# Performance work log

Measured on AMD Instinct MI355X. Metric: run time of the kernel, lower is better.

## Reference

```python
import jax, jax.numpy as jnp
import numpy as np

B, S, D = 2, 2048, 2048
H, KVH = 32, 8
HD = D // H          # 64
N_REP = H // KVH     # 4
NEG = -1e9


def setup_inputs() -> dict:
    key = jax.random.key(0)
    ks = jax.random.split(key, 5)
    x = jax.random.normal(ks[0], (B, S, D), dtype=jnp.float32)
    std = 0.02
    wq = jax.random.normal(ks[1], (H * HD, D), dtype=jnp.float32) * std
    wk = jax.random.normal(ks[2], (KVH * HD, D), dtype=jnp.float32) * std
    wv = jax.random.normal(ks[3], (KVH * HD, D), dtype=jnp.float32) * std
    wo = jax.random.normal(ks[4], (D, H * HD), dtype=jnp.float32) * std
    # RoPE tables: (S, HD//2)
    inv_freq = 1.0 / (10000.0 ** (np.arange(0, HD, 2, dtype=np.float32) / HD))
    t = np.arange(S, dtype=np.float32)
    freqs = np.outer(t, inv_freq)
    freqs_cos = jnp.asarray(np.cos(freqs))
    freqs_sin = jnp.asarray(np.sin(freqs))
    # additive causal mask [1,1,S,S]
    causal = np.tril(np.ones((S, S), dtype=bool))
    mask = jnp.asarray(np.where(causal, 0.0, NEG).astype(np.float32))[None, None]
    return {"x": x, "wq": wq, "wk": wk, "wv": wv, "wo": wo,
            "freqs_cos": freqs_cos, "freqs_sin": freqs_sin, "mask": mask}


def _apply_rope(t, cos, sin):
    # t: [B,S,nh,HD]; cos/sin: [S, HD//2]
    tr = t.reshape(t.shape[:-1] + (HD // 2, 2))
    r, i = tr[..., 0], tr[..., 1]
    c = cos[None, :, None, :]
    s = sin[None, :, None, :]
    out_r = r * c - i * s
    out_i = r * s + i * c
    return jnp.stack([out_r, out_i], axis=-1).reshape(t.shape)


def reference(x, wq, wk, wv, wo, freqs_cos, freqs_sin, mask):
    b, s, _ = x.shape
    q = (x @ wq.T).reshape(b, s, H, HD)
    k = (x @ wk.T).reshape(b, s, KVH, HD)
    v = (x @ wv.T).reshape(b, s, KVH, HD)
    q = _apply_rope(q, freqs_cos, freqs_sin)
    k = _apply_rope(k, freqs_cos, freqs_sin)
    # repeat_kv (GQA expansion) then move heads forward: [B,H,S,HD]
    k = jnp.repeat(k, N_REP, axis=2)
    v = jnp.repeat(v, N_REP, axis=2)
    q = q.transpose(0, 2, 1, 3)
    k = k.transpose(0, 2, 1, 3)
    v = v.transpose(0, 2, 1, 3)
    scale = 1.0 / jnp.sqrt(jnp.float32(HD))
    scores = jnp.einsum("bhqd,bhkd->bhqk", q, k) * scale + mask[:, :, :s, :s]
    attn = jax.nn.softmax(scores, axis=-1)
    out = jnp.einsum("bhqk,bhkd->bhqd", attn, v)
    out = out.transpose(0, 2, 1, 3).reshape(b, s, H * HD)
    return out @ wo.T
```

## Files before the change

kernel.cpp:

```cpp
#include <hip/hip_runtime.h>
#include <hip/hip_bf16.h>
#include <stdint.h>


#define NEG_BIG (-1e9f)
#define SCALE_LOG2 0.18033688011112042f
#define DEFER_THR 10.0f

typedef __bf16 bf16x8 __attribute__((ext_vector_type(8)));
typedef float f32x4 __attribute__((ext_vector_type(4)));
typedef float f32x16 __attribute__((ext_vector_type(16)));
typedef uint16_t u16x8 __attribute__((ext_vector_type(8)));
typedef uint32_t u32x4 __attribute__((ext_vector_type(4)));

__device__ inline uint16_t f2bf(float x) {
    __hip_bfloat16 h = __float2bfloat16(x);
    return __builtin_bit_cast(uint16_t, h);
}
__device__ inline float bf2f(uint16_t u) {
    uint32_t t = (uint32_t)u << 16;
    return __builtin_bit_cast(float, t);
}

__device__ inline void async_cp16(const void* g, void* l) {
    __builtin_amdgcn_global_load_lds(
        (const __attribute__((address_space(1))) uint32_t*)g,
        (__attribute__((address_space(3))) uint32_t*)l,
        16 , 0 , 0 );
}

__global__ void cvt4(const float* __restrict__ in, uint16_t* __restrict__ out, int n4) {
    int i = blockIdx.x * blockDim.x + threadIdx.x;
    if (i >= n4) return;
    const float4 v = ((const float4*)in)[i];
    ushort4 o;
    o.x = f2bf(v.x); o.y = f2bf(v.y); o.z = f2bf(v.z); o.w = f2bf(v.w);
    ((ushort4*)out)[i] = o;
}

__global__ void build_wqkv(const float* __restrict__ wq, const float* __restrict__ wk,
                           const float* __restrict__ wv, uint16_t* __restrict__ out) {
    int i = blockIdx.x * blockDim.x + threadIdx.x;
    if (i >= (3072 * 2048) / 4) return;
    int e = i * 4;
    int row = e >> 11;
    int col = e & 2047;
    const float* src = (row < 2048) ? (wq + (long)row * 2048 + col)
                     : (row < 2560) ? (wk + (long)(row - 2048) * 2048 + col)
                                    : (wv + (long)(row - 2560) * 2048 + col);
    const float4 v = *(const float4*)src;
    ushort4 o;
    o.x = f2bf(v.x); o.y = f2bf(v.y); o.z = f2bf(v.z); o.w = f2bf(v.w);
    ((ushort4*)(out + e))[0] = o;
}

template <int BN, int OUT_BF16>
__global__ __launch_bounds__(512) void gemm256(const uint16_t* __restrict__ A,
                                               const uint16_t* __restrict__ Bw,
                                               void* __restrict__ Cout,
                                               int M, int N, int K) {
    constexpr int WN = BN / 4;
    constexpr int NF = WN / 16;
    constexpr int BROUNDS = BN / 64;

    __shared__ __align__(16) uint16_t As[2][256 * 64];
    __shared__ __align__(16) uint16_t Bs[2][BN * 64];

    const int n0 = blockIdx.x;
    const int colt = 2 * (n0 & 7) + ((n0 >> 3) >> 4);
    const int rowt = (n0 >> 3) & 15;
    const long row0 = (long)rowt * 256;
    const long col0 = (long)colt * BN;

    const int tid = threadIdx.x;
    const int l = tid & 63;
    const int w = tid >> 6;
    const int wmi = w >> 2;
    const int wni = w & 3;
    const int c = l & 15, g = l >> 4;

    f32x4 acc[8][NF] = {};

    auto STAGE = [&](int buf, int t) {
        const long k0 = (long)t * 64;
#pragma unroll
        for (int rr = 0; rr < 4; ++rr) {
            const int e = rr * 512 + tid;
            const int r = e >> 3;
            const int gs = (e & 7) ^ (r & 7);
            async_cp16(A + (row0 + r) * (long)K + k0 + gs * 8, &As[buf][e * 8]);
        }
#pragma unroll
        for (int rr = 0; rr < BROUNDS; ++rr) {
            const int e = rr * 512 + tid;
            const int r = e >> 3;
            const int gs = (e & 7) ^ (r & 7);
            async_cp16(Bw + (col0 + r) * (long)K + k0 + gs * 8, &Bs[buf][e * 8]);
        }
    };

    STAGE(0, 0);
    __syncthreads();

    const int nt = K / 64;
    for (int t = 0; t < nt; ++t) {
        const int cur = t & 1;
        if (t + 1 < nt) STAGE(cur ^ 1, t + 1);

#pragma unroll
        for (int kk = 0; kk < 2; ++kk) {
            bf16x8 bF[NF];
#pragma unroll
            for (int n = 0; n < NF; ++n) {
                const int rb = wni * WN + n * 16 + c;
                const int sp = ((kk * 4 + g) ^ (c & 7));
                bF[n] = *(const bf16x8*)&Bs[cur][rb * 64 + sp * 8];
            }
#pragma unroll
            for (int mh = 0; mh < 2; ++mh) {
                bf16x8 aF[4];
#pragma unroll
                for (int mm = 0; mm < 4; ++mm) {
                    const int ra = wmi * 128 + (mh * 4 + mm) * 16 + c;
                    const int sp = ((kk * 4 + g) ^ (c & 7));
                    aF[mm] = *(const bf16x8*)&As[cur][ra * 64 + sp * 8];
                }
                __builtin_amdgcn_s_setprio(1);
#pragma unroll
                for (int mm = 0; mm < 4; ++mm)
#pragma unroll
                    for (int n = 0; n < NF; ++n)
                        acc[mh * 4 + mm][n] = __builtin_amdgcn_mfma_f32_16x16x32_bf16(
                            aF[mm], bF[n], acc[mh * 4 + mm][n], 0, 0, 0);
                __builtin_amdgcn_s_setprio(0);
            }
        }
        if (t + 1 < nt) __syncthreads();
    }

#pragma unroll
    for (int m = 0; m < 8; ++m) {
        const long rg = row0 + wmi * 128 + m * 16 + g * 4;
#pragma unroll
        for (int n = 0; n < NF; ++n) {
            const long cg = col0 + wni * WN + n * 16 + c;
#pragma unroll
            for (int r = 0; r < 4; ++r) {
                float v = acc[m][n][r];
                if (OUT_BF16)
                    ((uint16_t*)Cout)[(rg + r) * (long)N + cg] = f2bf(v);
                else
                    ((float*)Cout)[(rg + r) * (long)N + cg] = v;
            }
        }
    }
}

__global__ void pack_kv(const uint16_t* __restrict__ qkv,
                        const float* __restrict__ cosT,
                        const float* __restrict__ sinT,
                        uint16_t* __restrict__ Kpk,
                        uint16_t* __restrict__ Vpk) {
    const int gw = (blockIdx.x * blockDim.x + threadIdx.x) >> 6;
    const int l = threadIdx.x & 63;
    const int lq = l & 31, hi = l >> 5;
    if (gw < 4096) {
        const int wid = gw;
        const int s = wid & 3;
        const int tile = (wid >> 2) & 63;
        const int bk = wid >> 8;
        const int b = bk >> 3, kvh = bk & 7;
        const int key = 32 * tile + lq;
        const uint16_t* src = qkv + (long)(b * 2048 + key) * 3072
                            + 2048 + kvh * 64 + 16 * s + 8 * hi;
        u16x8 v = *(const u16x8*)src;
        const int d2b = 8 * s + 4 * hi;
        u16x8 o;
#pragma unroll
        for (int p = 0; p < 4; ++p) {
            const float cc = cosT[key * 32 + d2b + p];
            const float ss = sinT[key * 32 + d2b + p];
            const float re = bf2f(v[2 * p]);
            const float im = bf2f(v[2 * p + 1]);
            o[2 * p]     = f2bf(re * cc - im * ss);
            o[2 * p + 1] = f2bf(re * ss + im * cc);
        }
        *(u16x8*)(Kpk + (((long)(bk * 64 + tile) * 4 + s) * 64 + l) * 8) = o;
    } else {
        const int wid = gw - 4096;
        const int s2 = wid & 1;
        const int nd = (wid >> 1) & 1;
        const int tile = (wid >> 2) & 63;
        const int bk = wid >> 8;
        const int b = bk >> 3, kvh = bk & 7;
        const int key0 = 32 * tile + 16 * s2 + 8 * hi;
        const uint16_t* src = qkv + (long)(b * 2048 + key0) * 3072
                            + 2560 + kvh * 64 + nd * 32 + lq;
        u16x8 v;
#pragma unroll
        for (int jj = 0; jj < 8; ++jj) v[jj] = src[(long)jj * 3072];
        *(u16x8*)(Vpk + ((((long)(bk * 64 + tile) * 2 + nd) * 2 + s2) * 64 + l) * 8) = v;
    }
}

__device__ inline void pack_pf(const float pr[16], bf16x8 pf[2]) {
    uint32_t wds[8];
#pragma unroll
    for (int m = 0; m < 8; ++m)
        wds[m] = (uint32_t)f2bf(pr[2 * m]) | ((uint32_t)f2bf(pr[2 * m + 1]) << 16);
    asm volatile("v_permlane32_swap_b32 %0, %1" : "+v"(wds[0]), "+v"(wds[2]));
    asm volatile("v_permlane32_swap_b32 %0, %1" : "+v"(wds[1]), "+v"(wds[3]));
    asm volatile("v_permlane32_swap_b32 %0, %1" : "+v"(wds[4]), "+v"(wds[6]));
    asm volatile("v_permlane32_swap_b32 %0, %1" : "+v"(wds[5]), "+v"(wds[7]));
    u32x4 pk0 = {wds[0], wds[1], wds[2], wds[3]};
    u32x4 pk1 = {wds[4], wds[5], wds[6], wds[7]};
    pf[0] = __builtin_bit_cast(bf16x8, pk0);
    pf[1] = __builtin_bit_cast(bf16x8, pk1);
}

__global__ __launch_bounds__(128) void attn_fwd(const uint16_t* __restrict__ qkv,
                                                const float* __restrict__ cosT,
                                                const float* __restrict__ sinT,
                                                const uint16_t* __restrict__ Kpk,
                                                const uint16_t* __restrict__ Vpk,
                                                uint16_t* __restrict__ outb) {
    const int bid = blockIdx.x;
    const int bhp = bid & 31;
    const int j = 63 - (bid >> 5);
    const int t0 = threadIdx.x;
    const int l = t0 & 63, ww = t0 >> 6;
    const int gh = 2 * bhp + ww;
    const int b = gh >> 5, h = gh & 31;
    const int kvh = h >> 2;
    const int bk = b * 8 + kvh;
    const int lq = l & 31, hi = l >> 5;
    const int q = 32 * j + lq;

    const uint16_t* qrow = qkv + (long)(b * 2048 + q) * 3072 + h * 64 + 8 * hi;
    bf16x8 qf[4];
#pragma unroll
    for (int s = 0; s < 4; ++s) {
        const u16x8 v = *(const u16x8*)(qrow + 16 * s);
        const int d2b = 8 * s + 4 * hi;
        u16x8 o;
#pragma unroll
        for (int p = 0; p < 4; ++p) {
            const float cc = cosT[q * 32 + d2b + p];
            const float ss = sinT[q * 32 + d2b + p];
            const float re = bf2f(v[2 * p]);
            const float im = bf2f(v[2 * p + 1]);
            o[2 * p]     = f2bf((re * cc - im * ss) * SCALE_LOG2);
            o[2 * p + 1] = f2bf((re * ss + im * cc) * SCALE_LOG2);
        }
        qf[s] = __builtin_bit_cast(bf16x8, o);
    }

    float m_run = -1e30f, l_run = 0.f;
    f32x16 accO[2] = {};

    const uint16_t* kbase = Kpk + (long)bk * 64 * 2048 + (long)l * 8;
    const uint16_t* vbase = Vpk + (long)bk * 64 * 2048 + (long)l * 8;
    const int nT = (j + 2) >> 1;

    for (int t = 0; t < nT; ++t) {
        bf16x8 kf[2][4];
#pragma unroll
        for (int u = 0; u < 2; ++u)
#pragma unroll
            for (int s = 0; s < 4; ++s)
                kf[u][s] = *(const bf16x8*)(kbase + (long)(2 * t + u) * 2048 + s * 512);

        f32x16 st0 = {}, st1 = {};
        __builtin_amdgcn_s_setprio(1);
#pragma unroll
        for (int s = 0; s < 4; ++s)
            st0 = __builtin_amdgcn_mfma_f32_32x32x16_bf16(kf[0][s], qf[s], st0, 0, 0, 0);
#pragma unroll
        for (int s = 0; s < 4; ++s)
            st1 = __builtin_amdgcn_mfma_f32_32x32x16_bf16(kf[1][s], qf[s], st1, 0, 0, 0);
        __builtin_amdgcn_s_setprio(0);

        bf16x8 vf[2][2][2];
#pragma unroll
        for (int u = 0; u < 2; ++u)
#pragma unroll
            for (int nd = 0; nd < 2; ++nd)
#pragma unroll
                for (int s2 = 0; s2 < 2; ++s2)
                    vf[u][nd][s2] = *(const bf16x8*)(vbase + (long)(2 * t + u) * 2048 + nd * 1024 + s2 * 512);

        if (t == nT - 1) {
            const int tq0 = lq + ((j - 2 * t) << 5) - 4 * hi;
            const int tq1 = tq0 - 32;
#pragma unroll
            for (int r = 0; r < 16; ++r) {
                const int kc = (r & 3) + 8 * (r >> 2);
                if (kc > tq0) st0[r] = NEG_BIG;
                if (kc > tq1) st1[r] = NEG_BIG;
            }
        }

        float mx[16];
#pragma unroll
        for (int r = 0; r < 16; ++r) mx[r] = fmaxf(st0[r], st1[r]);
#pragma unroll
        for (int off = 8; off; off >>= 1)
#pragma unroll
            for (int r = 0; r < 8; ++r)
                if (r < off) mx[r] = fmaxf(mx[r], mx[r + off]);
        const float vm = fmaxf(mx[0], __shfl_xor(mx[0], 32));

        if (!__all(vm - m_run <= DEFER_THR)) {
            const float mnew = fmaxf(m_run, vm);
            const float alpha = __builtin_amdgcn_exp2f(m_run - mnew);
            m_run = mnew;
            l_run *= alpha;
#pragma unroll
            for (int nd = 0; nd < 2; ++nd)
#pragma unroll
                for (int r = 0; r < 16; ++r) accO[nd][r] *= alpha;
        }

        float pr0[16], pr1[16], sm[8];
#pragma unroll
        for (int r = 0; r < 16; ++r) pr0[r] = __builtin_amdgcn_exp2f(st0[r] - m_run);
#pragma unroll
        for (int r = 0; r < 16; ++r) pr1[r] = __builtin_amdgcn_exp2f(st1[r] - m_run);
#pragma unroll
        for (int m = 0; m < 8; ++m)
            sm[m] = (pr0[2 * m] + pr0[2 * m + 1]) + (pr1[2 * m] + pr1[2 * m + 1]);
#pragma unroll
        for (int off = 4; off; off >>= 1)
#pragma unroll
            for (int r = 0; r < 4; ++r)
                if (r < off) sm[r] += sm[r + off];
        l_run += sm[0] + __shfl_xor(sm[0], 32);

        bf16x8 pf0[2], pf1[2];
        pack_pf(pr0, pf0);
        pack_pf(pr1, pf1);

        __builtin_amdgcn_s_setprio(1);
#pragma unroll
        for (int nd = 0; nd < 2; ++nd) {
            accO[nd] = __builtin_amdgcn_mfma_f32_32x32x16_bf16(vf[0][nd][0], pf0[0], accO[nd], 0, 0, 0);
            accO[nd] = __builtin_amdgcn_mfma_f32_32x32x16_bf16(vf[0][nd][1], pf0[1], accO[nd], 0, 0, 0);
            accO[nd] = __builtin_amdgcn_mfma_f32_32x32x16_bf16(vf[1][nd][0], pf1[0], accO[nd], 0, 0, 0);
            accO[nd] = __builtin_amdgcn_mfma_f32_32x32x16_bf16(vf[1][nd][1], pf1[1], accO[nd], 0, 0, 0);
        }
        __builtin_amdgcn_s_setprio(0);
    }

    const float invl = 1.0f / l_run;
    uint16_t* orow = outb + (long)(b * 2048 + q) * 2048 + h * 64 + 4 * hi;
#pragma unroll
    for (int nd = 0; nd < 2; ++nd)
#pragma unroll
        for (int m = 0; m < 4; ++m) {
            ushort4 o;
            o.x = f2bf(accO[nd][4 * m + 0] * invl);
            o.y = f2bf(accO[nd][4 * m + 1] * invl);
            o.z = f2bf(accO[nd][4 * m + 2] * invl);
            o.w = f2bf(accO[nd][4 * m + 3] * invl);
            *(ushort4*)(orow + nd * 32 + 8 * m) = o;
        }
}

extern "C" void kernel_launch(void* const* d_in, const int* in_sizes, int n_in,
                              void* d_out, int out_size, void* d_ws, size_t ws_size,
                              hipStream_t stream) {
    const float* x    = (const float*)d_in[0];
    const float* wq   = (const float*)d_in[1];
    const float* wk   = (const float*)d_in[2];
    const float* wv   = (const float*)d_in[3];
    const float* wo   = (const float*)d_in[4];
    const float* fcos = (const float*)d_in[5];
    const float* fsin = (const float*)d_in[6];
    float* out = (float*)d_out;

    uint8_t* ws = (uint8_t*)d_ws;
    const size_t MiB = 1048576;
    uint16_t* x_bf   = (uint16_t*)(ws);
    uint16_t* w_bf   = (uint16_t*)(ws + 16 * MiB);
    uint16_t* qkv_bf = (uint16_t*)(ws + 28 * MiB);
    uint16_t* att_bf = x_bf;
    uint16_t* Kpk    = (uint16_t*)(ws + 16 * MiB);
    uint16_t* Vpk    = (uint16_t*)(ws + 20 * MiB);
    uint16_t* wo_bf  = (uint16_t*)(ws + 16 * MiB);

    cvt4<<<(2097152 + 255) / 256, 256, 0, stream>>>(x, x_bf, 2097152);
    build_wqkv<<<(1572864 + 255) / 256, 256, 0, stream>>>(wq, wk, wv, w_bf);

    gemm256<192, 1><<<256, 512, 0, stream>>>(x_bf, w_bf, qkv_bf, 4096, 3072, 2048);

    pack_kv<<<2048, 256, 0, stream>>>(qkv_bf, fcos, fsin, Kpk, Vpk);

    attn_fwd<<<2048, 128, 0, stream>>>(qkv_bf, fcos, fsin, Kpk, Vpk, att_bf);

    cvt4<<<(1048576 + 255) / 256, 256, 0, stream>>>(wo, wo_bf, 1048576);
    gemm256<128, 0><<<256, 512, 0, stream>>>(att_bf, wo_bf, out, 4096, 2048, 2048);
}
```

Baseline: 204.0 us.

## Process two GQA query heads per wave to reuse K/V fragment loads

Each wave now handles two query heads that share the same KV head, so every K and V fragment loaded from global memory feeds twice as many MFMAs. The grid is halved and the block-to-tile mapping changes to a snake order over query tiles with heads grouped by KV head, which is meant to balance the causal workload and improve cache locality. The cost is roughly double the live accumulator and score registers per wave, which may lower occupancy or cause spills, and fewer blocks are available to fill the GPU.

Result: slower. 216.4 us (+6.1%).

```diff
diff --git a/kernel.cpp b/kernel.cpp
--- a/kernel.cpp
+++ b/kernel.cpp
@@ -225,38 +225,47 @@
                                                 const uint16_t* __restrict__ Vpk,
                                                 uint16_t* __restrict__ outb) {
     const int bid = blockIdx.x;
-    const int bhp = bid & 31;
-    const int j = 63 - (bid >> 5);
-    const int t0 = threadIdx.x;
-    const int l = t0 & 63, ww = t0 >> 6;
-    const int gh = 2 * bhp + ww;
-    const int b = gh >> 5, h = gh & 31;
-    const int kvh = h >> 2;
+    const int p = bid >> 4;
+    const int k4 = p >> 4, a = p & 15;
+    const int j = (3 - k4) * 16 + ((k4 & 1) ? a : (15 - a));
+    const int gh2 = bid & 15;
+    const int b = gh2 >> 3, kvh = gh2 & 7;
+    const int tid = threadIdx.x;
+    const int l = tid & 63, ww = tid >> 6;
+    const int h0 = 4 * kvh + 2 * ww;
     const int bk = b * 8 + kvh;
     const int lq = l & 31, hi = l >> 5;
     const int q = 32 * j + lq;
 
-    const uint16_t* qrow = qkv + (long)(b * 2048 + q) * 3072 + h * 64 + 8 * hi;
-    bf16x8 qf[4];
+    const uint16_t* qrowb = qkv + (long)(b * 2048 + q) * 3072 + 8 * hi;
+    bf16x8 qf[2][4];
 #pragma unroll
     for (int s = 0; s < 4; ++s) {
-        const u16x8 v = *(const u16x8*)(qrow + 16 * s);
         const int d2b = 8 * s + 4 * hi;
-        u16x8 o;
-#pragma unroll
-        for (int p = 0; p < 4; ++p) {
-            const float cc = cosT[q * 32 + d2b + p];
-            const float ss = sinT[q * 32 + d2b + p];
-            const float re = bf2f(v[2 * p]);
-            const float im = bf2f(v[2 * p + 1]);
-            o[2 * p]     = f2bf((re * cc - im * ss) * SCALE_LOG2);
-            o[2 * p + 1] = f2bf((re * ss + im * cc) * SCALE_LOG2);
-        }
-        qf[s] = __builtin_bit_cast(bf16x8, o);
-    }
-
-    float m_run = -1e30f, l_run = 0.f;
-    f32x16 accO[2] = {};
+        float cc[4], ss[4];
+#pragma unroll
+        for (int pp = 0; pp < 4; ++pp) {
+            cc[pp] = cosT[q * 32 + d2b + pp];
+            ss[pp] = sinT[q * 32 + d2b + pp];
+        }
+#pragma unroll
+        for (int hh = 0; hh < 2; ++hh) {
+            const u16x8 v = *(const u16x8*)(qrowb + (h0 + hh) * 64 + 16 * s);
+            u16x8 o;
+#pragma unroll
+            for (int pp = 0; pp < 4; ++pp) {
+                const float re = bf2f(v[2 * pp]);
+                const float im = bf2f(v[2 * pp + 1]);
+                o[2 * pp]     = f2bf((re * cc[pp] - im * ss[pp]) * SCALE_LOG2);
+                o[2 * pp + 1] = f2bf((re * ss[pp] + im * cc[pp]) * SCALE_LOG2);
+            }
+            qf[hh][s] = __builtin_bit_cast(bf16x8, o);
+        }
+    }
+
+    float m_run[2] = {-1e30f, -1e30f};
+    float l_run[2] = {0.f, 0.f};
+    f32x16 accO[2][2] = {};
 
     const uint16_t* kbase = Kpk + (long)bk * 64 * 2048 + (long)l * 8;
     const uint16_t* vbase = Vpk + (long)bk * 64 * 2048 + (long)l * 8;
@@ -270,14 +279,20 @@
             for (int s = 0; s < 4; ++s)
                 kf[u][s] = *(const bf16x8*)(kbase + (long)(2 * t + u) * 2048 + s * 512);
 
-        f32x16 st0 = {}, st1 = {};
+        f32x16 st[2][2];
         __builtin_amdgcn_s_setprio(1);
 #pragma unroll
-        for (int s = 0; s < 4; ++s)
-            st0 = __builtin_amdgcn_mfma_f32_32x32x16_bf16(kf[0][s], qf[s], st0, 0, 0, 0);
-#pragma unroll
-        for (int s = 0; s < 4; ++s)
-            st1 = __builtin_amdgcn_mfma_f32_32x32x16_bf16(kf[1][s], qf[s], st1, 0, 0, 0);
+        for (int hh = 0; hh < 2; ++hh) {
+            f32x16 z0 = {}, z1 = {};
+#pragma unroll
+            for (int s = 0; s < 4; ++s)
+                z0 = __builtin_amdgcn_mfma_f32_32x32x16_bf16(kf[0][s], qf[hh][s], z0, 0, 0, 0);
+#pragma unroll
+            for (int s = 0; s < 4; ++s)
+                z1 = __builtin_amdgcn_mfma_f32_32x32x16_bf16(kf[1][s], qf[hh][s], z1, 0, 0, 0);
+            st[hh][0] = z0;
+            st[hh][1] = z1;
+        }
         __builtin_amdgcn_s_setprio(0);
 
         bf16x8 vf[2][2][2];
@@ -295,75 +310,84 @@
 #pragma unroll
             for (int r = 0; r < 16; ++r) {
                 const int kc = (r & 3) + 8 * (r >> 2);
-                if (kc > tq0) st0[r] = NEG_BIG;
-                if (kc > tq1) st1[r] = NEG_BIG;
-            }
-        }
-
-        float mx[16];
-#pragma unroll
-        for (int r = 0; r < 16; ++r) mx[r] = fmaxf(st0[r], st1[r]);
-#pragma unroll
-        for (int off = 8; off; off >>= 1)
-#pragma unroll
-            for (int r = 0; r < 8; ++r)
-                if (r < off) mx[r] = fmaxf(mx[r], mx[r + off]);
-        const float vm = fmaxf(mx[0], __shfl_xor(mx[0], 32));
-
-        if (!__all(vm - m_run <= DEFER_THR)) {
-            const float mnew = fmaxf(m_run, vm);
-            const float alpha = __builtin_amdgcn_exp2f(m_run - mnew);
-            m_run = mnew;
-            l_run *= alpha;
-#pragma unroll
-            for (int nd = 0; nd < 2; ++nd)
-#pragma unroll
-                for (int r = 0; r < 16; ++r) accO[nd][r] *= alpha;
-        }
-
-        float pr0[16], pr1[16], sm[8];
-#pragma unroll
-        for (int r = 0; r < 16; ++r) pr0[r] = __builtin_amdgcn_exp2f(st0[r] - m_run);
-#pragma unroll
-        for (int r = 0; r < 16; ++r) pr1[r] = __builtin_amdgcn_exp2f(st1[r] - m_run);
-#pragma unroll
-        for (int m = 0; m < 8; ++m)
-            sm[m] = (pr0[2 * m] + pr0[2 * m + 1]) + (pr1[2 * m] + pr1[2 * m + 1]);
-#pragma unroll
-        for (int off = 4; off; off >>= 1)
-#pragma unroll
-            for (int r = 0; r < 4; ++r)
-                if (r < off) sm[r] += sm[r + off];
-        l_run += sm[0] + __shfl_xor(sm[0], 32);
-
-        bf16x8 pf0[2], pf1[2];
-        pack_pf(pr0, pf0);
-        pack_pf(pr1, pf1);
-
-        __builtin_amdgcn_s_setprio(1);
-#pragma unroll
-        for (int nd = 0; nd < 2; ++nd) {
-            accO[nd] = __builtin_amdgcn_mfma_f32_32x32x16_bf16(vf[0][nd][0], pf0[0], accO[nd], 0, 0, 0);
-            accO[nd] = __builtin_amdgcn_mfma_f32_32x32x16_bf16(vf[0][nd][1], pf0[1], accO[nd], 0, 0, 0);
-            accO[nd] = __builtin_amdgcn_mfma_f32_32x32x16_bf16(vf[1][nd][0], pf1[0], accO[nd], 0, 0, 0);
-            accO[nd] = __builtin_amdgcn_mfma_f32_32x32x16_bf16(vf[1][nd][1], pf1[1], accO[nd], 0, 0, 0);
-        }
-        __builtin_amdgcn_s_setprio(0);
-    }
-
-    const float invl = 1.0f / l_run;
-    uint16_t* orow = outb + (long)(b * 2048 + q) * 2048 + h * 64 + 4 * hi;
-#pragma unroll
-    for (int nd = 0; nd < 2; ++nd)
-#pragma unroll
-        for (int m = 0; m < 4; ++m) {
-            ushort4 o;
-            o.x = f2bf(accO[nd][4 * m + 0] * invl);
-            o.y = f2bf(accO[nd][4 * m + 1] * invl);
-            o.z = f2bf(accO[nd][4 * m + 2] * invl);
-            o.w = f2bf(accO[nd][4 * m + 3] * invl);
-            *(ushort4*)(orow + nd * 32 + 8 * m) = o;
-        }
+#pragma unroll
+                for (int hh = 0; hh < 2; ++hh) {
+                    if (kc > tq0) st[hh][0][r] = NEG_BIG;
+                    if (kc > tq1) st[hh][1][r] = NEG_BIG;
+                }
+            }
+        }
+
+#pragma unroll
+        for (int hh = 0; hh < 2; ++hh) {
+            float mx[16];
+#pragma unroll
+            for (int r = 0; r < 16; ++r) mx[r] = fmaxf(st[hh][0][r], st[hh][1][r]);
+#pragma unroll
+            for (int off = 8; off; off >>= 1)
+#pragma unroll
+                for (int r = 0; r < 8; ++r)
+                    if (r < off) mx[r] = fmaxf(mx[r], mx[r + off]);
+            const float vm = fmaxf(mx[0], __shfl_xor(mx[0], 32));
+
+            if (!__all(vm - m_run[hh] <= DEFER_THR)) {
+                const float mnew = fmaxf(m_run[hh], vm);
+                const float alpha = __builtin_amdgcn_exp2f(m_run[hh] - mnew);
+                m_run[hh] = mnew;
+                l_run[hh] *= alpha;
+#pragma unroll
+                for (int nd = 0; nd < 2; ++nd)
+#pragma unroll
+                    for (int r = 0; r < 16; ++r) accO[hh][nd][r] *= alpha;
+            }
+
+            float pr0[16], pr1[16], sm[8];
+#pragma unroll
+            for (int r = 0; r < 16; ++r) pr0[r] = __builtin_amdgcn_exp2f(st[hh][0][r] - m_run[hh]);
+#pragma unroll
+            for (int r = 0; r < 16; ++r) pr1[r] = __builtin_amdgcn_exp2f(st[hh][1][r] - m_run[hh]);
+#pragma unroll
+            for (int m = 0; m < 8; ++m)
+                sm[m] = (pr0[2 * m] + pr0[2 * m + 1]) + (pr1[2 * m] + pr1[2 * m + 1]);
+#pragma unroll
+            for (int off = 4; off; off >>= 1)
+#pragma unroll
+                for (int r = 0; r < 4; ++r)
+                    if (r < off) sm[r] += sm[r + off];
+            l_run[hh] += sm[0] + __shfl_xor(sm[0], 32);
+
+            bf16x8 pf0[2], pf1[2];
+            pack_pf(pr0, pf0);
+            pack_pf(pr1, pf1);
+
+            __builtin_amdgcn_s_setprio(1);
+#pragma unroll
+            for (int nd = 0; nd < 2; ++nd) {
+                accO[hh][nd] = __builtin_amdgcn_mfma_f32_32x32x16_bf16(vf[0][nd][0], pf0[0], accO[hh][nd], 0, 0, 0);
+                accO[hh][nd] = __builtin_amdgcn_mfma_f32_32x32x16_bf16(vf[0][nd][1], pf0[1], accO[hh][nd], 0, 0, 0);
+                accO[hh][nd] = __builtin_amdgcn_mfma_f32_32x32x16_bf16(vf[1][nd][0], pf1[0], accO[hh][nd], 0, 0, 0);
+                accO[hh][nd] = __builtin_amdgcn_mfma_f32_32x32x16_bf16(vf[1][nd][1], pf1[1], accO[hh][nd], 0, 0, 0);
+            }
+            __builtin_amdgcn_s_setprio(0);
+        }
+    }
+
+#pragma unroll
+    for (int hh = 0; hh < 2; ++hh) {
+        const float invl = 1.0f / l_run[hh];
+        uint16_t* orow = outb + (long)(b * 2048 + q) * 2048 + (h0 + hh) * 64 + 4 * hi;
+#pragma unroll
+        for (int nd = 0; nd < 2; ++nd)
+#pragma unroll
+            for (int m = 0; m < 4; ++m) {
+                ushort4 o;
+                o.x = f2bf(accO[hh][nd][4 * m + 0] * invl);
+                o.y = f2bf(accO[hh][nd][4 * m + 1] * invl);
+                o.z = f2bf(accO[hh][nd][4 * m + 2] * invl);
+                o.w = f2bf(accO[hh][nd][4 * m + 3] * invl);
+                *(ushort4*)(orow + nd * 32 + 8 * m) = o;
+            }
+    }
 }
 
 extern "C" void kernel_launch(void* const* d_in, const int* in_sizes, int n_in,
@@ -395,7 +419,7 @@
 
     pack_kv<<<2048, 256, 0, stream>>>(qkv_bf, fcos, fsin, Kpk, Vpk);
 
-    attn_fwd<<<2048, 128, 0, stream>>>(qkv_bf, fcos, fsin, Kpk, Vpk, att_bf);
+    attn_fwd<<<1024, 128, 0, stream>>>(qkv_bf, fcos, fsin, Kpk, Vpk, att_bf);
 
     cvt4<<<(1048576 + 255) / 256, 256, 0, stream>>>(wo, wo_bf, 1048576);
     gemm256<128, 0><<<256, 512, 0, stream>>>(att_bf, wo_bf, out, 4096, 2048, 2048);
```
